# Kernel tuning notes

Hardware: AMD Instinct MI355X
Metric: run time of the kernel (lower is better)

Reference implementation:

```python
import jax, jax.numpy as jnp
import numpy as np

B = 1024      # batch
M = 4096      # num_meas
W = 2         # width_per_meas
L = 2         # num_hidden_layers
Z = 64        # num_vae_latent
H = M * W     # hidden_dim = 8192


def setup_inputs() -> dict:
    key = jax.random.key(0)
    ks = jax.random.split(key, 24)

    def nrm(i, shape, scale=0.02):
        return (jax.random.normal(ks[i], shape, dtype=jnp.float32) * scale)

    return {
        "x": jax.random.normal(ks[0], (B, M), dtype=jnp.float32),
        "eps": jax.random.normal(ks[1], (B, Z), dtype=jnp.float32),
        # encoder (dense)
        "enc1_w": nrm(2, (M, M)), "enc1_b": nrm(3, (M,)),
        "enc2_w": nrm(4, (M, M)), "enc2_b": nrm(5, (M,)),
        "mu_w": nrm(6, (Z, M)), "mu_b": nrm(7, (Z,)),
        "lv_w": nrm(8, (Z, M)), "lv_b": nrm(9, (Z,)),
        # decoder mean branch: fulcon dense, hidden/output in block form
        "mean_ful_w": nrm(10, (H, Z)), "mean_ful_b": nrm(11, (H,)),
        "mean_h_w": nrm(12, (L, M, W, W)), "mean_h_b": nrm(13, (L, H)),
        "mean_out_w": nrm(14, (M, W)), "mean_out_b": nrm(15, (M,)),
        # decoder logcov branch
        "cov_ful_w": nrm(16, (H, Z)), "cov_ful_b": nrm(17, (H,)),
        "cov_h_w": nrm(18, (L, M, W, W)), "cov_h_b": nrm(19, (L, H)),
        "cov_out_w": nrm(20, (M, W)), "cov_out_b": nrm(21, (M,)),
    }


def _decoder_branch(z, ful_w, ful_b, h_w, h_b, out_w, out_b):
    # fulcon: dense latent -> hidden, then sigmoid
    a = jax.nn.sigmoid(z @ ful_w.T + ful_b)            # [B, H]
    a = a.reshape(B, M, W)                             # block-diag structure
    for l in range(L):
        # grouped block-diagonal matmul == masked dense linear of the original
        a = jax.nn.sigmoid(
            jnp.einsum('bmw,mvw->bmv', a, h_w[l]) + h_b[l].reshape(M, W)
        )
    # output mask blocks are [1, W] per measurement
    return jnp.einsum('bmw,mw->bm', a, out_w) + out_b  # [B, M]


def reference(x, eps, enc1_w, enc1_b, enc2_w, enc2_b, mu_w, mu_b, lv_w, lv_b,
              mean_ful_w, mean_ful_b, mean_h_w, mean_h_b, mean_out_w, mean_out_b,
              cov_ful_w, cov_ful_b, cov_h_w, cov_h_b, cov_out_w, cov_out_b):
    # encoder
    h = jax.nn.relu(x @ enc1_w.T + enc1_b)
    h = jax.nn.relu(h @ enc2_w.T + enc2_b)
    mu = h @ mu_w.T + mu_b
    logvar = h @ lv_w.T + lv_b
    # reparameterization (training mode, eps supplied)
    z = mu + jnp.exp(0.5 * logvar) * eps
    # decoder
    x_recon = _decoder_branch(z, mean_ful_w, mean_ful_b, mean_h_w, mean_h_b,
                              mean_out_w, mean_out_b)
    logcov = _decoder_branch(z, cov_ful_w, cov_ful_b, cov_h_w, cov_h_b,
                             cov_out_w, cov_out_b)
    return (x_recon, logcov, mu, logvar)
```

## Files before the change

kernel.cpp:

```cpp
#include <hip/hip_runtime.h>
#include <hip/hip_bf16.h>
#include <stdint.h>

typedef __hip_bfloat16 bf16;
typedef __bf16 bf16x8 __attribute__((ext_vector_type(8)));
typedef float f32x4 __attribute__((ext_vector_type(4)));

#define NB 1024
#define NM 4096
#define NZ 64
#define NH 8192

__device__ __forceinline__ float bf2f(bf16 x) { return __bfloat162float(x); }
__device__ __forceinline__ bf16 f2bf(float x) { return __float2bfloat16(x); }
__device__ __forceinline__ float sigf(float x) { return 1.f / (1.f + __expf(-x)); }

__global__ __launch_bounds__(256) void cvt_f32_bf16(const float* __restrict__ src,
                                                    bf16* __restrict__ dst, int n4) {
  const int i = blockIdx.x * 256 + threadIdx.x;
  if (i >= n4) return;
  const float4 v = ((const float4*)src)[i];
  bf16 o[4] = {f2bf(v.x), f2bf(v.y), f2bf(v.z), f2bf(v.w)};
  *(short4*)&dst[i * 4] = *(short4*)o;
}

__global__ void zero_f32(float* p, int n) {
  int i = blockIdx.x * blockDim.x + threadIdx.x;
  if (i < n) p[i] = 0.f;
}

#define VMW4 asm volatile("s_waitcnt vmcnt(4)" ::: "memory")
#define VMW0 asm volatile("s_waitcnt vmcnt(0)" ::: "memory")
#define LGKM0 asm volatile("s_waitcnt lgkmcnt(0)" ::: "memory")

__global__ __launch_bounds__(512) void gemm_nt(const bf16* __restrict__ A,
                                               const float* __restrict__ W,
                                               const float* __restrict__ bias,
                                               bf16* __restrict__ C,
                                               int K, int N) {
  __shared__ __attribute__((aligned(16))) bf16 smA[3][128 * 64];
  __shared__ __attribute__((aligned(16))) bf16 smB[2][64 * 64];
  const int tid  = threadIdx.x;
  const int lane = tid & 63;
  const int w    = tid >> 6;
  const int wr   = w >> 1;
  const int wc   = w & 1;

  const int lid  = blockIdx.y * 8 + blockIdx.x;
  const int wgid = (lid & 7) * 64 + (lid >> 3);
  const int row0 = (wgid & 7) * 128;
  const int col0 = (wgid >> 3) * 64;

  f32x4 acc[2][2];
#pragma unroll
  for (int i = 0; i < 2; i++)
#pragma unroll
    for (int j = 0; j < 2; j++) acc[i][j] = (f32x4){0.f, 0.f, 0.f, 0.f};

  const int swr = tid >> 3;
  const int swk = (tid & 7) * 8;
  const float* wp = W + (size_t)(col0 + swr) * K + swk;
  const int woff = swr * 64 + (swk ^ ((swr & 7) << 3));

  auto load_W = [&](float4 (&wv)[2], int kk) {
    wv[0] = *(const float4*)(wp + kk);
    wv[1] = *(const float4*)(wp + kk + 4);
  };

  auto stage_A = [&](int slot, int kk) {
#pragma unroll
    for (int q = 0; q < 2; q++) {
      const int chunk = q * 512 + w * 64 + lane;
      const int r  = chunk >> 3;
      const int ke = ((chunk & 7) ^ (r & 7)) * 8;
      __builtin_amdgcn_global_load_lds(
          (__attribute__((address_space(1))) unsigned int*)(A + (size_t)(row0 + r) * K + (kk + ke)),
          (__attribute__((address_space(3))) unsigned int*)(&smA[slot][(q * 512 + w * 64) * 8]),
          16, 0, 0);
    }
  };

  auto write_W = [&](int slot, const float4 (&wv)[2]) {
    bf16 t[8] = {f2bf(wv[0].x), f2bf(wv[0].y), f2bf(wv[0].z), f2bf(wv[0].w),
                 f2bf(wv[1].x), f2bf(wv[1].y), f2bf(wv[1].z), f2bf(wv[1].w)};
    *(bf16x8*)&smB[slot][woff] = *(bf16x8*)t;
  };

  auto compute = [&](int sa, int ws) {
#pragma unroll
    for (int ks = 0; ks < 64; ks += 32) {
      const int kq = ks + (lane >> 4) * 8;
      bf16x8 af[2], bfr[2];
#pragma unroll
      for (int i = 0; i < 2; i++) {
        const int r = wr * 32 + i * 16 + (lane & 15);
        af[i] = *(const bf16x8*)&smA[sa][r * 64 + (kq ^ ((r & 7) << 3))];
      }
#pragma unroll
      for (int j = 0; j < 2; j++) {
        const int r = wc * 32 + j * 16 + (lane & 15);
        bfr[j] = *(const bf16x8*)&smB[ws][r * 64 + (kq ^ ((r & 7) << 3))];
      }
#pragma unroll
      for (int i = 0; i < 2; i++)
#pragma unroll
        for (int j = 0; j < 2; j++)
          acc[i][j] = __builtin_amdgcn_mfma_f32_16x16x32_bf16(af[i], bfr[j], acc[i][j], 0, 0, 0);
    }
  };

  const int K64 = K >> 6;
  float4 wA[2], wB[2];

  load_W(wA, 0);
  stage_A(0, 0);
  asm volatile("" ::: "memory");
  load_W(wB, 64);
  stage_A(1, 64);

  int sa = 0;
  for (int i = 0; i + 2 < K64; i += 2) {
    const int nx  = (sa + 1 == 3) ? 0 : sa + 1;
    const int nnx = (nx + 1 == 3) ? 0 : nx + 1;
    VMW4;
    write_W(0, wA);
    LGKM0;
    __builtin_amdgcn_s_barrier();
    __builtin_amdgcn_sched_barrier(0);
    load_W(wA, (i + 2) * 64);
    stage_A(nnx, (i + 2) * 64);
    compute(sa, 0);
    VMW4;
    write_W(1, wB);
    LGKM0;
    __builtin_amdgcn_s_barrier();
    __builtin_amdgcn_sched_barrier(0);
    load_W(wB, (i + 3) * 64);
    stage_A(sa, (i + 3) * 64);
    compute(nx, 1);
    sa = nnx;
  }
  VMW4;
  write_W(0, wA);
  LGKM0;
  __builtin_amdgcn_s_barrier();
  __builtin_amdgcn_sched_barrier(0);
  compute(sa, 0);
  VMW0;
  write_W(1, wB);
  LGKM0;
  __builtin_amdgcn_s_barrier();
  __builtin_amdgcn_sched_barrier(0);
  compute((sa + 1 == 3) ? 0 : sa + 1, 1);

#pragma unroll
  for (int i = 0; i < 2; i++) {
#pragma unroll
    for (int j = 0; j < 2; j++) {
      const int cc = col0 + wc * 32 + j * 16 + (lane & 15);
      const float bs = bias[cc];
#pragma unroll
      for (int t = 0; t < 4; t++) {
        const int rr = row0 + wr * 32 + i * 16 + (lane >> 4) * 4 + t;
        float v = acc[i][j][t] + bs;
        v = v > 0.f ? v : 0.f;
        C[(size_t)rr * N + cc] = f2bf(v);
      }
    }
  }
}

__global__ __launch_bounds__(256) void mulv_splitk(const bf16* __restrict__ h2,
                                                   const float* __restrict__ muw,
                                                   const float* __restrict__ lvw,
                                                   float* __restrict__ zpre) {
  __shared__ float sA[32][33];
  __shared__ float sW[32][128];
  const int tid = threadIdx.x;
  const int b0 = blockIdx.x * 32;
  const int k0 = blockIdx.y * 256;
  const int tj = tid & 15;
  const int tb = tid >> 4;
  float acc[2][8];
#pragma unroll
  for (int i = 0; i < 2; i++)
#pragma unroll
    for (int j = 0; j < 8; j++) acc[i][j] = 0.f;

  const int lb = tid >> 3, lk = (tid & 7) * 4;
  const int wj = tid >> 1, wk = (tid & 1) * 16;
  const float* wrow = (wj < 64) ? (muw + (size_t)wj * NM) : (lvw + (size_t)(wj - 64) * NM);

  for (int kc = 0; kc < 256; kc += 32) {
    __syncthreads();
    {
      const uint2 v = *(const uint2*)(h2 + (size_t)(b0 + lb) * NM + (k0 + kc + lk));
      sA[lk + 0][lb] = __uint_as_float(v.x << 16);
      sA[lk + 1][lb] = __uint_as_float(v.x & 0xffff0000u);
      sA[lk + 2][lb] = __uint_as_float(v.y << 16);
      sA[lk + 3][lb] = __uint_as_float(v.y & 0xffff0000u);
      const float* q = wrow + (k0 + kc + wk);
#pragma unroll
      for (int i = 0; i < 4; i++) {
        const float4 f = *(const float4*)(q + i * 4);
        sW[wk + i * 4 + 0][wj] = f.x;
        sW[wk + i * 4 + 1][wj] = f.y;
        sW[wk + i * 4 + 2][wj] = f.z;
        sW[wk + i * 4 + 3][wj] = f.w;
      }
    }
    __syncthreads();
#pragma unroll
    for (int k = 0; k < 32; k++) {
      const float av0 = sA[k][tb * 2 + 0];
      const float av1 = sA[k][tb * 2 + 1];
      float wv[8];
#pragma unroll
      for (int j = 0; j < 8; j++) wv[j] = sW[k][16 * j + tj];
#pragma unroll
      for (int j = 0; j < 8; j++) {
        acc[0][j] += av0 * wv[j];
        acc[1][j] += av1 * wv[j];
      }
    }
  }
#pragma unroll
  for (int i = 0; i < 2; i++)
#pragma unroll
    for (int j = 0; j < 8; j++)
      atomicAdd(&zpre[(size_t)(b0 + tb * 2 + i) * 128 + 16 * j + tj], acc[i][j]);
}

__global__ void zfin(const float* __restrict__ zpre, const float* __restrict__ eps,
                     const float* __restrict__ mub, const float* __restrict__ lvb,
                     float* __restrict__ out_mu, float* __restrict__ out_lv,
                     float* __restrict__ z) {
  const int i = blockIdx.x * 256 + threadIdx.x;
  const int b = i >> 6, j = i & 63;
  const float mu = zpre[(size_t)b * 128 + j] + mub[j];
  const float lv = zpre[(size_t)b * 128 + 64 + j] + lvb[j];
  const float zz = mu + expf(0.5f * lv) * eps[i];
  out_mu[i] = mu;
  out_lv[i] = lv;
  z[i] = zz;
}

__global__ __launch_bounds__(256) void dec_fused(
    const float* __restrict__ z,
    const float* __restrict__ fw, const float* __restrict__ fb,
    const float* __restrict__ hw, const float* __restrict__ hb,
    const float* __restrict__ ow, const float* __restrict__ ob,
    float* __restrict__ out) {
  __shared__ __attribute__((aligned(16))) float sZ[64][68];
  __shared__ __attribute__((aligned(16))) float sFW[32][132];
  const int tid = threadIdx.x;
  const int b0 = blockIdx.x * 64;
  const int m0 = blockIdx.y * 256;
  const int mi = blockIdx.z;
  {
    const int r  = tid >> 2;
    const int c0 = (tid & 3) * 16;
    const float* p = z + (size_t)(b0 + r) * NZ + c0;
#pragma unroll
    for (int i = 0; i < 16; i++) sZ[c0 + i][r] = p[i];
  }

  const int bq = tid >> 5;
  const int tm = tid & 31;
  const int mb = m0 + mi * 64;
  const int mA = mb + 2 * tm;

  const float4 fb4 = *(const float4*)&fb[2 * mA];
  float aA0[8], aA1[8], aB0[8], aB1[8];
#pragma unroll
  for (int j = 0; j < 8; j++) { aA0[j] = fb4.x; aA1[j] = fb4.y; aB0[j] = fb4.z; aB1[j] = fb4.w; }

  const int R0 = 2 * mb;
#pragma unroll
  for (int kh = 0; kh < 2; kh++) {
    __syncthreads();
    {
#pragma unroll
      for (int q = 0; q < 4; q++) {
        const int v = tid + q * 256;
        const int grow = v >> 3;
        const int gk = (v & 7) * 4;
        const float4 f4 = *(const float4*)&fw[(size_t)(R0 + grow) * NZ + kh * 32 + gk];
        sFW[gk + 0][grow] = f4.x;
        sFW[gk + 1][grow] = f4.y;
        sFW[gk + 2][grow] = f4.z;
        sFW[gk + 3][grow] = f4.w;
      }
    }
    __syncthreads();

#pragma unroll 8
    for (int k2 = 0; k2 < 32; k2++) {
      const int k = kh * 32 + k2;
      const float4 w4 = *(const float4*)&sFW[k2][4 * tm];
      const float4 z0 = *(const float4*)&sZ[k][bq * 8 + 0];
      const float4 z1 = *(const float4*)&sZ[k][bq * 8 + 4];
      const float zv[8] = {z0.x, z0.y, z0.z, z0.w, z1.x, z1.y, z1.z, z1.w};
#pragma unroll
      for (int j = 0; j < 8; j++) {
        aA0[j] += zv[j] * w4.x;
        aA1[j] += zv[j] * w4.y;
        aB0[j] += zv[j] * w4.z;
        aB1[j] += zv[j] * w4.w;
      }
    }
  }

  float4 hwA[2], hwB[2], hb4[2];
#pragma unroll
  for (int l = 0; l < 2; l++) {
    hwA[l] = *(const float4*)&hw[((size_t)l * NM + mA) * 4];
    hwB[l] = *(const float4*)&hw[((size_t)l * NM + mA) * 4 + 4];
    hb4[l] = *(const float4*)&hb[(size_t)l * NH + 2 * mA];
  }
  const float4 o4 = *(const float4*)&ow[2 * mA];
  const float2 ob2 = *(const float2*)&ob[mA];
#pragma unroll
  for (int j = 0; j < 8; j++) {
    float a0 = sigf(aA0[j]), a1 = sigf(aA1[j]);
    float b0v = sigf(aB0[j]), b1v = sigf(aB1[j]);
#pragma unroll
    for (int l = 0; l < 2; l++) {
      const float nA0 = sigf(hwA[l].x * a0 + hwA[l].y * a1 + hb4[l].x);
      const float nA1 = sigf(hwA[l].z * a0 + hwA[l].w * a1 + hb4[l].y);
      const float nB0 = sigf(hwB[l].x * b0v + hwB[l].y * b1v + hb4[l].z);
      const float nB1 = sigf(hwB[l].z * b0v + hwB[l].w * b1v + hb4[l].w);
      a0 = nA0; a1 = nA1; b0v = nB0; b1v = nB1;
    }
    const float outA = a0 * o4.x + a1 * o4.y + ob2.x;
    const float outB = b0v * o4.z + b1v * o4.w + ob2.y;
    float2 o2; o2.x = outA; o2.y = outB;
    *(float2*)&out[(size_t)(b0 + bq * 8 + j) * NM + mA] = o2;
  }
}

extern "C" void kernel_launch(void* const* d_in, const int* in_sizes, int n_in,
                              void* d_out, int out_size, void* d_ws, size_t ws_size,
                              hipStream_t stream) {
  const float* x   = (const float*)d_in[0];
  const float* eps = (const float*)d_in[1];
  const float* e1w = (const float*)d_in[2];
  const float* e1b = (const float*)d_in[3];
  const float* e2w = (const float*)d_in[4];
  const float* e2b = (const float*)d_in[5];
  const float* muw = (const float*)d_in[6];
  const float* mub = (const float*)d_in[7];
  const float* lvw = (const float*)d_in[8];
  const float* lvb = (const float*)d_in[9];
  const float* mfw = (const float*)d_in[10];
  const float* mfb = (const float*)d_in[11];
  const float* mhw = (const float*)d_in[12];
  const float* mhb = (const float*)d_in[13];
  const float* mow = (const float*)d_in[14];
  const float* mob = (const float*)d_in[15];
  const float* cfw = (const float*)d_in[16];
  const float* cfb = (const float*)d_in[17];
  const float* chw = (const float*)d_in[18];
  const float* chb = (const float*)d_in[19];
  const float* cow = (const float*)d_in[20];
  const float* cob = (const float*)d_in[21];

  char* ob_ = (char*)d_out;
  float* out_x  = (float*)ob_;
  float* out_lc = (float*)(ob_ + (16u << 20));
  float* out_mu = out_x + (size_t)2 * NB * NM;
  float* out_lv = out_mu + (size_t)NB * NZ;
  bf16* h1 = (bf16*)ob_;
  bf16* xb = (bf16*)(ob_ + (16u << 20));
  bf16* h2 = xb;

  float* zpre = (float*)d_ws;
  float* z    = (float*)((char*)d_ws + (1u << 19));

  cvt_f32_bf16<<<dim3(4096), 256, 0, stream>>>(x, xb, NB * NM / 4);
  zero_f32<<<dim3(512), 256, 0, stream>>>(zpre, NB * 128);
  gemm_nt<<<dim3(8, 64), 512, 0, stream>>>(xb, e1w, e1b, h1, NM, NM);
  gemm_nt<<<dim3(8, 64), 512, 0, stream>>>(h1, e2w, e2b, h2, NM, NM);
  mulv_splitk<<<dim3(32, 16), 256, 0, stream>>>(h2, muw, lvw, zpre);
  zfin<<<dim3(256), 256, 0, stream>>>(zpre, eps, mub, lvb, out_mu, out_lv, z);
  dec_fused<<<dim3(16, 16, 4), 256, 0, stream>>>(z, mfw, mfb, mhw, mhb, mow, mob, out_x);
  dec_fused<<<dim3(16, 16, 4), 256, 0, stream>>>(z, cfw, cfb, chw, chb, cow, cob, out_lc);
}
```

Baseline: 426.4 us.

## Retile encoder GEMM to 64x64 blocks and move mu/logvar projection to MFMA

```diff
diff --git a/kernel.cpp b/kernel.cpp
--- a/kernel.cpp
+++ b/kernel.cpp
@@ -29,16 +29,27 @@
   if (i < n) p[i] = 0.f;
 }
 
+__global__ __launch_bounds__(256) void wcat_build(const float* __restrict__ muw,
+                                                  const float* __restrict__ lvw,
+                                                  float* __restrict__ wcat) {
+  const int v = blockIdx.x * 256 + threadIdx.x;
+  const int j = v >> 10;
+  const int k4 = v & 1023;
+  const float* src = (j < 64) ? (muw + (size_t)j * NM) : (lvw + (size_t)(j - 64) * NM);
+  ((float4*)(wcat + (size_t)j * NM))[k4] = ((const float4*)src)[k4];
+}
+
+#define VMW6 asm volatile("s_waitcnt vmcnt(6)" ::: "memory")
 #define VMW4 asm volatile("s_waitcnt vmcnt(4)" ::: "memory")
 #define VMW0 asm volatile("s_waitcnt vmcnt(0)" ::: "memory")
 #define LGKM0 asm volatile("s_waitcnt lgkmcnt(0)" ::: "memory")
 
-__global__ __launch_bounds__(512) void gemm_nt(const bf16* __restrict__ A,
+__global__ __launch_bounds__(256) void gemm_nt(const bf16* __restrict__ A,
                                                const float* __restrict__ W,
                                                const float* __restrict__ bias,
                                                bf16* __restrict__ C,
                                                int K, int N) {
-  __shared__ __attribute__((aligned(16))) bf16 smA[3][128 * 64];
+  __shared__ __attribute__((aligned(16))) bf16 smA[3][64 * 64];
   __shared__ __attribute__((aligned(16))) bf16 smB[2][64 * 64];
   const int tid  = threadIdx.x;
   const int lane = tid & 63;
@@ -46,10 +57,10 @@
   const int wr   = w >> 1;
   const int wc   = w & 1;
 
-  const int lid  = blockIdx.y * 8 + blockIdx.x;
-  const int wgid = (lid & 7) * 64 + (lid >> 3);
-  const int row0 = (wgid & 7) * 128;
-  const int col0 = (wgid >> 3) * 64;
+  const int lid  = blockIdx.y * 16 + blockIdx.x;
+  const int wgid = (lid & 7) * 128 + (lid >> 3);
+  const int row0 = (wgid & 15) * 64;
+  const int col0 = (wgid >> 4) * 64;
 
   f32x4 acc[2][2];
 #pragma unroll
@@ -57,33 +68,40 @@
 #pragma unroll
     for (int j = 0; j < 2; j++) acc[i][j] = (f32x4){0.f, 0.f, 0.f, 0.f};
 
-  const int swr = tid >> 3;
-  const int swk = (tid & 7) * 8;
+  const int swr = tid >> 2;
+  const int swk = (tid & 3) * 16;
   const float* wp = W + (size_t)(col0 + swr) * K + swk;
-  const int woff = swr * 64 + (swk ^ ((swr & 7) << 3));
-
-  auto load_W = [&](float4 (&wv)[2], int kk) {
+  const int swz = (swr & 7) << 3;
+  const int woff0 = swr * 64 + ((swk + 0) ^ swz);
+  const int woff1 = swr * 64 + ((swk + 8) ^ swz);
+
+  auto load_W = [&](float4 (&wv)[4], int kk) {
     wv[0] = *(const float4*)(wp + kk);
     wv[1] = *(const float4*)(wp + kk + 4);
+    wv[2] = *(const float4*)(wp + kk + 8);
+    wv[3] = *(const float4*)(wp + kk + 12);
   };
 
   auto stage_A = [&](int slot, int kk) {
 #pragma unroll
     for (int q = 0; q < 2; q++) {
-      const int chunk = q * 512 + w * 64 + lane;
+      const int chunk = q * 256 + w * 64 + lane;
       const int r  = chunk >> 3;
       const int ke = ((chunk & 7) ^ (r & 7)) * 8;
       __builtin_amdgcn_global_load_lds(
           (__attribute__((address_space(1))) unsigned int*)(A + (size_t)(row0 + r) * K + (kk + ke)),
-          (__attribute__((address_space(3))) unsigned int*)(&smA[slot][(q * 512 + w * 64) * 8]),
+          (__attribute__((address_space(3))) unsigned int*)(&smA[slot][(q * 256 + w * 64) * 8]),
           16, 0, 0);
     }
   };
 
-  auto write_W = [&](int slot, const float4 (&wv)[2]) {
-    bf16 t[8] = {f2bf(wv[0].x), f2bf(wv[0].y), f2bf(wv[0].z), f2bf(wv[0].w),
-                 f2bf(wv[1].x), f2bf(wv[1].y), f2bf(wv[1].z), f2bf(wv[1].w)};
-    *(bf16x8*)&smB[slot][woff] = *(bf16x8*)t;
+  auto write_W = [&](int slot, const float4 (&wv)[4]) {
+    bf16 t[16] = {f2bf(wv[0].x), f2bf(wv[0].y), f2bf(wv[0].z), f2bf(wv[0].w),
+                  f2bf(wv[1].x), f2bf(wv[1].y), f2bf(wv[1].z), f2bf(wv[1].w),
+                  f2bf(wv[2].x), f2bf(wv[2].y), f2bf(wv[2].z), f2bf(wv[2].w),
+                  f2bf(wv[3].x), f2bf(wv[3].y), f2bf(wv[3].z), f2bf(wv[3].w)};
+    *(bf16x8*)&smB[slot][woff0] = ((bf16x8*)t)[0];
+    *(bf16x8*)&smB[slot][woff1] = ((bf16x8*)t)[1];
   };
 
   auto compute = [&](int sa, int ws) {
@@ -110,7 +128,7 @@
   };
 
   const int K64 = K >> 6;
-  float4 wA[2], wB[2];
+  float4 wA[4], wB[4];
 
   load_W(wA, 0);
   stage_A(0, 0);
@@ -122,7 +140,7 @@
   for (int i = 0; i + 2 < K64; i += 2) {
     const int nx  = (sa + 1 == 3) ? 0 : sa + 1;
     const int nnx = (nx + 1 == 3) ? 0 : nx + 1;
-    VMW4;
+    VMW6;
     write_W(0, wA);
     LGKM0;
     __builtin_amdgcn_s_barrier();
@@ -130,7 +148,7 @@
     load_W(wA, (i + 2) * 64);
     stage_A(nnx, (i + 2) * 64);
     compute(sa, 0);
-    VMW4;
+    VMW6;
     write_W(1, wB);
     LGKM0;
     __builtin_amdgcn_s_barrier();
@@ -140,7 +158,7 @@
     compute(nx, 1);
     sa = nnx;
   }
-  VMW4;
+  VMW6;
   write_W(0, wA);
   LGKM0;
   __builtin_amdgcn_s_barrier();
@@ -170,65 +188,130 @@
   }
 }
 
-__global__ __launch_bounds__(256) void mulv_splitk(const bf16* __restrict__ h2,
-                                                   const float* __restrict__ muw,
-                                                   const float* __restrict__ lvw,
-                                                   float* __restrict__ zpre) {
-  __shared__ float sA[32][33];
-  __shared__ float sW[32][128];
-  const int tid = threadIdx.x;
-  const int b0 = blockIdx.x * 32;
-  const int k0 = blockIdx.y * 256;
-  const int tj = tid & 15;
-  const int tb = tid >> 4;
-  float acc[2][8];
+__global__ __launch_bounds__(512) void mulv_mfma(const bf16* __restrict__ A,
+                                                 const float* __restrict__ Wc,
+                                                 float* __restrict__ zpre) {
+  __shared__ __attribute__((aligned(16))) bf16 smA[3][128 * 64];
+  __shared__ __attribute__((aligned(16))) bf16 smB[2][64 * 64];
+  const int tid  = threadIdx.x;
+  const int lane = tid & 63;
+  const int w    = tid >> 6;
+  const int wr   = w >> 1;
+  const int wc   = w & 1;
+  const int row0 = blockIdx.x * 128;
+  const int col0 = blockIdx.y * 64;
+  const int k0g  = blockIdx.z * 256;
+
+  f32x4 acc[2][2];
 #pragma unroll
   for (int i = 0; i < 2; i++)
 #pragma unroll
-    for (int j = 0; j < 8; j++) acc[i][j] = 0.f;
-
-  const int lb = tid >> 3, lk = (tid & 7) * 4;
-  const int wj = tid >> 1, wk = (tid & 1) * 16;
-  const float* wrow = (wj < 64) ? (muw + (size_t)wj * NM) : (lvw + (size_t)(wj - 64) * NM);
-
-  for (int kc = 0; kc < 256; kc += 32) {
-    __syncthreads();
-    {
-      const uint2 v = *(const uint2*)(h2 + (size_t)(b0 + lb) * NM + (k0 + kc + lk));
-      sA[lk + 0][lb] = __uint_as_float(v.x << 16);
-      sA[lk + 1][lb] = __uint_as_float(v.x & 0xffff0000u);
-      sA[lk + 2][lb] = __uint_as_float(v.y << 16);
-      sA[lk + 3][lb] = __uint_as_float(v.y & 0xffff0000u);
-      const float* q = wrow + (k0 + kc + wk);
-#pragma unroll
-      for (int i = 0; i < 4; i++) {
-        const float4 f = *(const float4*)(q + i * 4);
-        sW[wk + i * 4 + 0][wj] = f.x;
-        sW[wk + i * 4 + 1][wj] = f.y;
-        sW[wk + i * 4 + 2][wj] = f.z;
-        sW[wk + i * 4 + 3][wj] = f.w;
-      }
-    }
-    __syncthreads();
-#pragma unroll
-    for (int k = 0; k < 32; k++) {
-      const float av0 = sA[k][tb * 2 + 0];
-      const float av1 = sA[k][tb * 2 + 1];
-      float wv[8];
-#pragma unroll
-      for (int j = 0; j < 8; j++) wv[j] = sW[k][16 * j + tj];
-#pragma unroll
-      for (int j = 0; j < 8; j++) {
-        acc[0][j] += av0 * wv[j];
-        acc[1][j] += av1 * wv[j];
-      }
-    }
-  }
-#pragma unroll
-  for (int i = 0; i < 2; i++)
-#pragma unroll
-    for (int j = 0; j < 8; j++)
-      atomicAdd(&zpre[(size_t)(b0 + tb * 2 + i) * 128 + 16 * j + tj], acc[i][j]);
+    for (int j = 0; j < 2; j++) acc[i][j] = (f32x4){0.f, 0.f, 0.f, 0.f};
+
+  const int swr = tid >> 3;
+  const int swk = (tid & 7) * 8;
+  const float* wp = Wc + (size_t)(col0 + swr) * NM + k0g + swk;
+  const int woff = swr * 64 + (swk ^ ((swr & 7) << 3));
+
+  auto load_W = [&](float4 (&wv)[2], int kk) {
+    wv[0] = *(const float4*)(wp + kk);
+    wv[1] = *(const float4*)(wp + kk + 4);
+  };
+
+  auto stage_A = [&](int slot, int kk) {
+#pragma unroll
+    for (int q = 0; q < 2; q++) {
+      const int chunk = q * 512 + w * 64 + lane;
+      const int r  = chunk >> 3;
+      const int ke = ((chunk & 7) ^ (r & 7)) * 8;
+      __builtin_amdgcn_global_load_lds(
+          (__attribute__((address_space(1))) unsigned int*)(A + (size_t)(row0 + r) * NM + (k0g + kk + ke)),
+          (__attribute__((address_space(3))) unsigned int*)(&smA[slot][(q * 512 + w * 64) * 8]),
+          16, 0, 0);
+    }
+  };
+
+  auto write_W = [&](int slot, const float4 (&wv)[2]) {
+    bf16 t[8] = {f2bf(wv[0].x), f2bf(wv[0].y), f2bf(wv[0].z), f2bf(wv[0].w),
+                 f2bf(wv[1].x), f2bf(wv[1].y), f2bf(wv[1].z), f2bf(wv[1].w)};
+    *(bf16x8*)&smB[slot][woff] = *(bf16x8*)t;
+  };
+
+  auto compute = [&](int sa, int ws) {
+#pragma unroll
+    for (int ks = 0; ks < 64; ks += 32) {
+      const int kq = ks + (lane >> 4) * 8;
+      bf16x8 af[2], bfr[2];
+#pragma unroll
+      for (int i = 0; i < 2; i++) {
+        const int r = wr * 32 + i * 16 + (lane & 15);
+        af[i] = *(const bf16x8*)&smA[sa][r * 64 + (kq ^ ((r & 7) << 3))];
+      }
+#pragma unroll
+      for (int j = 0; j < 2; j++) {
+        const int r = wc * 32 + j * 16 + (lane & 15);
+        bfr[j] = *(const bf16x8*)&smB[ws][r * 64 + (kq ^ ((r & 7) << 3))];
+      }
+#pragma unroll
+      for (int i = 0; i < 2; i++)
+#pragma unroll
+        for (int j = 0; j < 2; j++)
+          acc[i][j] = __builtin_amdgcn_mfma_f32_16x16x32_bf16(af[i], bfr[j], acc[i][j], 0, 0, 0);
+    }
+  };
+
+  float4 wA[2], wB[2];
+  load_W(wA, 0);
+  stage_A(0, 0);
+  asm volatile("" ::: "memory");
+  load_W(wB, 64);
+  stage_A(1, 64);
+
+  int sa = 0;
+  {
+    VMW4;
+    write_W(0, wA);
+    LGKM0;
+    __builtin_amdgcn_s_barrier();
+    __builtin_amdgcn_sched_barrier(0);
+    load_W(wA, 128);
+    stage_A(2, 128);
+    compute(0, 0);
+    VMW4;
+    write_W(1, wB);
+    LGKM0;
+    __builtin_amdgcn_s_barrier();
+    __builtin_amdgcn_sched_barrier(0);
+    load_W(wB, 192);
+    stage_A(0, 192);
+    compute(1, 1);
+    sa = 2;
+  }
+  VMW4;
+  write_W(0, wA);
+  LGKM0;
+  __builtin_amdgcn_s_barrier();
+  __builtin_amdgcn_sched_barrier(0);
+  compute(2, 0);
+  VMW0;
+  write_W(1, wB);
+  LGKM0;
+  __builtin_amdgcn_s_barrier();
+  __builtin_amdgcn_sched_barrier(0);
+  compute(0, 1);
+
+#pragma unroll
+  for (int i = 0; i < 2; i++) {
+#pragma unroll
+    for (int j = 0; j < 2; j++) {
+      const int cc = col0 + wc * 32 + j * 16 + (lane & 15);
+#pragma unroll
+      for (int t = 0; t < 4; t++) {
+        const int rr = row0 + wr * 32 + i * 16 + (lane >> 4) * 4 + t;
+        atomicAdd(&zpre[(size_t)rr * 128 + cc], acc[i][j][t]);
+      }
+    }
+  }
 }
 
 __global__ void zfin(const float* __restrict__ zpre, const float* __restrict__ eps,
@@ -373,15 +456,17 @@
   bf16* h1 = (bf16*)ob_;
   bf16* xb = (bf16*)(ob_ + (16u << 20));
   bf16* h2 = xb;
+  float* wcat = (float*)(ob_ + (24u << 20));
 
   float* zpre = (float*)d_ws;
   float* z    = (float*)((char*)d_ws + (1u << 19));
 
   cvt_f32_bf16<<<dim3(4096), 256, 0, stream>>>(x, xb, NB * NM / 4);
   zero_f32<<<dim3(512), 256, 0, stream>>>(zpre, NB * 128);
-  gemm_nt<<<dim3(8, 64), 512, 0, stream>>>(xb, e1w, e1b, h1, NM, NM);
-  gemm_nt<<<dim3(8, 64), 512, 0, stream>>>(h1, e2w, e2b, h2, NM, NM);
-  mulv_splitk<<<dim3(32, 16), 256, 0, stream>>>(h2, muw, lvw, zpre);
+  wcat_build<<<dim3(512), 256, 0, stream>>>(muw, lvw, wcat);
+  gemm_nt<<<dim3(16, 64), 256, 0, stream>>>(xb, e1w, e1b, h1, NM, NM);
+  gemm_nt<<<dim3(16, 64), 256, 0, stream>>>(h1, e2w, e2b, h2, NM, NM);
+  mulv_mfma<<<dim3(8, 2, 16), 512, 0, stream>>>(h2, wcat, zpre);
   zfin<<<dim3(256), 256, 0, stream>>>(zpre, eps, mub, lvb, out_mu, out_lv, z);
   dec_fused<<<dim3(16, 16, 4), 256, 0, stream>>>(z, mfw, mfb, mhw, mhb, mow, mob, out_x);
   dec_fused<<<dim3(16, 16, 4), 256, 0, stream>>>(z, cfw, cfb, chw, chb, cow, cob, out_lc);
```

After: 461.5 us. 1.08x slower.
